# Kernel tuning notes

Measured on AMD Instinct MI355X. Metric: run time of the kernel, lower is better.

Reference implementation:

```python
import jax, jax.numpy as jnp
import numpy as np

SEQ, VOCAB, HID, OUT = 8192, 256, 2048, 256


def setup_inputs() -> dict:
    key = jax.random.key(0)
    ks = jax.random.split(key, 21)
    def lin(kw, fan_in, shape):
        return (jax.random.normal(kw, shape, dtype=jnp.float32) / np.sqrt(fan_in)).astype(jnp.float32)
    inp = {
        "x": jax.random.randint(ks[0], (SEQ, 1), 0, VOCAB, dtype=jnp.int64 if jax.config.read("jax_enable_x64") else jnp.int32),
        "emb": jax.random.normal(ks[1], (VOCAB, VOCAB), dtype=jnp.float32),
        "W_i": lin(ks[2], VOCAB, (VOCAB, HID)), "b_i": lin(ks[3], VOCAB, (HID,)),
        "U_i": lin(ks[4], HID, (HID, HID)),   "c_i": lin(ks[5], HID, (HID,)),
        "W_f": lin(ks[6], VOCAB, (VOCAB, HID)), "b_f": lin(ks[7], VOCAB, (HID,)),
        "U_f": lin(ks[8], HID, (HID, HID)),   "c_f": lin(ks[9], HID, (HID,)),
        "W_g": lin(ks[10], VOCAB, (VOCAB, HID)), "b_g": lin(ks[11], VOCAB, (HID,)),
        "U_g": lin(ks[12], HID, (HID, HID)),  "c_g": lin(ks[13], HID, (HID,)),
        "W_o": lin(ks[14], VOCAB, (VOCAB, HID)), "b_o": lin(ks[15], VOCAB, (HID,)),
        "U_o": lin(ks[16], HID, (HID, HID)),  "c_o": lin(ks[17], HID, (HID,)),
        "V_w": lin(ks[18], HID, (HID, OUT)),  "V_b": lin(ks[19], HID, (OUT,)),
    }
    return inp


def reference(x, emb, W_i, b_i, U_i, c_i, W_f, b_f, U_f, c_f,
              W_g, b_g, U_g, c_g, W_o, b_o, U_o, c_o, V_w, V_b):
    H = U_i.shape[0]
    # embedding lookup: (S,1) ids -> (S,1,V)
    x_emb = emb[x[:, 0]][:, None, :]
    # precompute all input projections (the W_* matmuls are time-independent)
    gi = x_emb @ W_i + b_i  # (S,1,H)
    gf = x_emb @ W_f + b_f
    gg = x_emb @ W_g + b_g
    go = x_emb @ W_o + b_o

    def step(carry, gates):
        h, c = carry  # (1,H) each
        zi, zf, zg, zo = gates
        i = jax.nn.sigmoid(zi + h @ U_i + c_i)
        f = jax.nn.sigmoid(zf + h @ U_f + c_f)
        g = jnp.tanh(zg + h @ U_g + c_g)
        o = jax.nn.sigmoid(zo + h @ U_o + c_o)
        c_new = f * c + i * g
        h_new = o * jnp.tanh(c_new)
        return (h_new, c_new), h_new

    h0 = jnp.zeros((1, H), dtype=x_emb.dtype)
    c0 = jnp.zeros((1, H), dtype=x_emb.dtype)
    (h_T, c_T), hs = jax.lax.scan(step, (h0, c0), (gi, gf, gg, go))
    out = hs @ V_w + V_b  # (S,1,OUT)
    return out, (jax.lax.stop_gradient(h_T), jax.lax.stop_gradient(c_T))
```

## Files before the change

kernel.cpp:

```cpp
#include <hip/hip_runtime.h>

#define SEQ   8192
#define VOCAB 256
#define HID   2048
#define ODIM  256
#define NBLK  256
#define NTHR  512
#define JPB   8

typedef unsigned int v4u __attribute__((ext_vector_type(4)));

__device__ __forceinline__ void ld32_coh_sync(const void* p, v4u& r0, v4u& r1) {
    asm volatile("global_load_dwordx4 %0, %2, off sc0 sc1\n\t"
                 "global_load_dwordx4 %1, %2, off offset:16 sc0 sc1\n\t"
                 "s_waitcnt vmcnt(0)"
                 : "=&v"(r0), "=&v"(r1) : "v"(p) : "memory");
}

__device__ __forceinline__ float fsigmoid(float x) {
    return __builtin_amdgcn_rcpf(1.f + __expf(-x));
}
__device__ __forceinline__ float ftanh(float x) {
    x = fminf(20.f, fmaxf(-20.f, x));
    float e = __expf(2.f * x);
    return (e - 1.f) * __builtin_amdgcn_rcpf(e + 1.f);
}

__device__ __forceinline__ float dpp_ror4(float v) {
    return __int_as_float(__builtin_amdgcn_update_dpp(
        0, __float_as_int(v), 0x124, 0xF, 0xF, false));
}
__device__ __forceinline__ float dpp_ror8(float v) {
    return __int_as_float(__builtin_amdgcn_update_dpp(
        0, __float_as_int(v), 0x128, 0xF, 0xF, false));
}

__global__ void k_zv(const float* __restrict__ emb, const float* __restrict__ W,
                     const float* __restrict__ bb, const float* __restrict__ cb,
                     float* __restrict__ Zv, int gate) {
    __shared__ float e[32][VOCAB];
    const int tid = threadIdx.x;
    const int vt = blockIdx.x, ct = blockIdx.y;
    for (int r = 0; r < 32; ++r)
        e[r][tid] = emb[(size_t)(vt * 32 + r) * VOCAB + tid];
    __syncthreads();
    const int j = ct * 256 + tid;
    const float bias = bb[j] + cb[j];
    float acc[32];
#pragma unroll
    for (int r = 0; r < 32; ++r) acc[r] = 0.f;
    for (int u = 0; u < VOCAB; ++u) {
        float w = W[(size_t)u * HID + j];
#pragma unroll
        for (int r = 0; r < 32; ++r) acc[r] += e[r][u] * w;
    }
    for (int r = 0; r < 32; ++r)
        Zv[(size_t)(vt * 32 + r) * (4 * HID) + (size_t)gate * HID + j] = acc[r] + bias;
}

__launch_bounds__(NTHR, 2)
__global__ void k_lstm(const float* __restrict__ Uii, const float* __restrict__ Uff,
                       const float* __restrict__ Ugg, const float* __restrict__ Uoo,
                       const float* __restrict__ Zv,  const int* __restrict__ x,
                       unsigned long long* pub, float* __restrict__ hs,
                       float* __restrict__ outTail) {
    __shared__ __align__(16) float hpad[128 * 20];
    __shared__ __align__(16) float scr2[2][32 * 36];

    const int tid  = threadIdx.x;
    const int b    = blockIdx.x;
    const int gate = tid & 3;
    const int rs   = tid >> 2;
    const int lane = tid & 63;
    const int wv   = tid >> 6;
    const int jg   = b * JPB + wv;

    const float* Ug = (gate == 0) ? Uii : (gate == 1) ? Uff : (gate == 2) ? Ugg : Uoo;

    float u[16][JPB];
#pragma unroll
    for (int r = 0; r < 16; ++r) {
        const float4* p = (const float4*)(Ug + (size_t)(rs * 16 + r) * HID + b * JPB);
        float4 a0 = p[0], a1 = p[1];
        u[r][0] = a0.x; u[r][1] = a0.y; u[r][2] = a0.z; u[r][3] = a0.w;
        u[r][4] = a1.x; u[r][5] = a1.y; u[r][6] = a1.z; u[r][7] = a1.w;
    }

    float4* hp4 = (float4*)hpad;
    float creg = 0.f;
    unsigned budget = 1u << 22;

    for (int t = 0; t < SEQ; ++t) {
        const int xt = x[t];
        float zx = Zv[(size_t)xt * (4 * HID) + (size_t)gate * HID + jg];

        float4 hv;
        if (t == 0) {
            hv = make_float4(0.f, 0.f, 0.f, 0.f);
        } else {
            const unsigned tgt = (unsigned)t;
            const unsigned long long* sl = pub + (size_t)(t & 1) * HID + tid * 4;
            v4u A0, A1;
            for (;;) {
                ld32_coh_sync(sl, A0, A1);
                if (((A0.y == tgt) & (A0.w == tgt) &
                     (A1.y == tgt) & (A1.w == tgt)) || budget == 0) break;
                --budget;
                __builtin_amdgcn_s_sleep(1);
            }
            hv.x = __uint_as_float(A0.x);
            hv.y = __uint_as_float(A0.z);
            hv.z = __uint_as_float(A1.x);
            hv.w = __uint_as_float(A1.z);
        }

        *(float4*)&hpad[(tid >> 2) * 20 + (tid & 3) * 4] = hv;
        __threadfence_block();

        float acc[JPB];
#pragma unroll
        for (int jj = 0; jj < JPB; ++jj) acc[jj] = 0.f;
#pragma unroll
        for (int k = 0; k < 4; ++k) {
            float4 h4 = hp4[rs * 5 + k];
            float hvv[4] = {h4.x, h4.y, h4.z, h4.w};
#pragma unroll
            for (int i = 0; i < 4; ++i)
#pragma unroll
                for (int jj = 0; jj < JPB; ++jj)
                    acc[jj] += hvv[i] * u[k * 4 + i][jj];
        }

#pragma unroll
        for (int jj = 0; jj < JPB; ++jj) {
            acc[jj] += dpp_ror4(acc[jj]);
            acc[jj] += dpp_ror8(acc[jj]);
        }
        if ((lane & 12) == 0) {
            const int chunk = wv * 4 + (lane >> 4);
            float* p = &scr2[t & 1][chunk * 36 + gate * JPB];
            *(float4*)(p)     = make_float4(acc[0], acc[1], acc[2], acc[3]);
            *(float4*)(p + 4) = make_float4(acc[4], acc[5], acc[6], acc[7]);
        }
        __syncthreads();

        {
            const int c = lane >> 2;
            const float* s = &scr2[t & 1][0];
            float z = s[c * 36 + gate * JPB + wv] +
                      s[(c + 16) * 36 + gate * JPB + wv];
            z += __shfl_xor(z, 4);
            z += __shfl_xor(z, 8);
            z += __shfl_xor(z, 16);
            z += __shfl_xor(z, 32);
            z += zx;
            float zi = __shfl(z, 0);
            float zf = __shfl(z, 1);
            float zg = __shfl(z, 2);
            float zo = __shfl(z, 3);
            float ig = fsigmoid(zi);
            float fg = fsigmoid(zf);
            float gg = ftanh(zg);
            float og = fsigmoid(zo);
            float cn = fg * creg + ig * gg;
            float hn = og * ftanh(cn);
            creg = cn;
            if (lane == 0) {
                unsigned long long pk =
                    ((unsigned long long)(unsigned)(t + 1) << 32) | __float_as_uint(hn);
                __hip_atomic_store(&pub[(size_t)((t + 1) & 1) * HID + jg], pk,
                                   __ATOMIC_RELAXED, __HIP_MEMORY_SCOPE_AGENT);
                hs[(size_t)t * HID + jg] = hn;
                if (t == SEQ - 1) { outTail[jg] = hn; outTail[HID + jg] = cn; }
            }
        }
    }
}

__global__ void k_out(const float* __restrict__ hs, const float* __restrict__ Vw,
                      const float* __restrict__ Vb, float* __restrict__ out) {
    __shared__ float tile[32][64];
    const int tid = threadIdx.x;
    const int t0 = blockIdx.x * 32;
    float acc[32];
#pragma unroll
    for (int r = 0; r < 32; ++r) acc[r] = 0.f;
    for (int k0 = 0; k0 < HID; k0 += 64) {
        {
            const int r = tid >> 3, kk = (tid & 7) * 8;
            const float4* p = (const float4*)(hs + (size_t)(t0 + r) * HID + k0 + kk);
            float4 a = p[0], bq = p[1];
            *(float4*)&tile[r][kk]     = a;
            *(float4*)&tile[r][kk + 4] = bq;
        }
        __syncthreads();
        for (int kk = 0; kk < 64; ++kk) {
            float w = Vw[(size_t)(k0 + kk) * ODIM + tid];
#pragma unroll
            for (int r = 0; r < 32; ++r) acc[r] += tile[r][kk] * w;
        }
        __syncthreads();
    }
    const float vb = Vb[tid];
    for (int r = 0; r < 32; ++r)
        out[(size_t)(t0 + r) * ODIM + tid] = acc[r] + vb;
}

extern "C" void kernel_launch(void* const* d_in, const int* in_sizes, int n_in,
                              void* d_out, int out_size, void* d_ws, size_t ws_size,
                              hipStream_t stream) {
    const int*   x   = (const int*)d_in[0];
    const float* emb = (const float*)d_in[1];
    const float* W[4] = {(const float*)d_in[2], (const float*)d_in[6],
                         (const float*)d_in[10], (const float*)d_in[14]};
    const float* B[4] = {(const float*)d_in[3], (const float*)d_in[7],
                         (const float*)d_in[11], (const float*)d_in[15]};
    const float* U[4] = {(const float*)d_in[4], (const float*)d_in[8],
                         (const float*)d_in[12], (const float*)d_in[16]};
    const float* C[4] = {(const float*)d_in[5], (const float*)d_in[9],
                         (const float*)d_in[13], (const float*)d_in[17]};
    const float* Vw = (const float*)d_in[18];
    const float* Vb = (const float*)d_in[19];
    float* out = (float*)d_out;

    float* ws = (float*)d_ws;
    float* Zv = ws;
    float* hs = Zv + (size_t)VOCAB * 4 * HID;
    unsigned long long* pub = (unsigned long long*)(hs + (size_t)SEQ * HID);

    for (int g = 0; g < 4; ++g)
        k_zv<<<dim3(8, 8), dim3(256), 0, stream>>>(emb, W[g], B[g], C[g], Zv, g);

    float* outTail = out + (size_t)SEQ * ODIM;
    const float *Ui = U[0], *Uf = U[1], *Ugp = U[2], *Uo = U[3];
    const float* Zvc = Zv; const int* xc = x;
    unsigned long long* pubc = pub; float* hsc = hs; float* ot = outTail;
    void* args[9] = {&Ui, &Uf, &Ugp, &Uo, &Zvc, &xc, &pubc, &hsc, &ot};
    hipLaunchCooperativeKernel((void*)k_lstm, dim3(NBLK), dim3(NTHR), args, 0, stream);

    k_out<<<dim3(256), dim3(256), 0, stream>>>(hs, Vw, Vb, out);
}
```

Baseline: 17.60 ms.

## Split publish slots into two halves and poll each half independently

Rearranges the per-step published hidden-state slots so each reader thread's four values sit in two 16-byte chunks in separate halves of the buffer, written by different waves. The spin loop now re-polls only the chunk that is still stale instead of reloading all 32 bytes, and alternates probes when both are stale. The intent is to cut coherent-load traffic and latency in the cross-block synchronisation of the sequential LSTM recurrence. In exchange the polling loop has more branching and the slot index mapping is harder to follow.

```diff
diff --git a/kernel.cpp b/kernel.cpp
--- a/kernel.cpp
+++ b/kernel.cpp
@@ -10,11 +10,18 @@
 
 typedef unsigned int v4u __attribute__((ext_vector_type(4)));
 
-__device__ __forceinline__ void ld32_coh_sync(const void* p, v4u& r0, v4u& r1) {
+__device__ __forceinline__ void ld16_coh_sync(const void* p, v4u& r) {
+    asm volatile("global_load_dwordx4 %0, %1, off sc0 sc1\n\t"
+                 "s_waitcnt vmcnt(0)"
+                 : "=&v"(r) : "v"(p) : "memory");
+}
+
+__device__ __forceinline__ void ld32_2q(const void* pE, const void* pO,
+                                        v4u& r0, v4u& r1) {
     asm volatile("global_load_dwordx4 %0, %2, off sc0 sc1\n\t"
-                 "global_load_dwordx4 %1, %2, off offset:16 sc0 sc1\n\t"
+                 "global_load_dwordx4 %1, %3, off sc0 sc1\n\t"
                  "s_waitcnt vmcnt(0)"
-                 : "=&v"(r0), "=&v"(r1) : "v"(p) : "memory");
+                 : "=&v"(r0), "=&v"(r1) : "v"(pE), "v"(pO) : "memory");
 }
 
 __device__ __forceinline__ float fsigmoid(float x) {
@@ -86,6 +93,8 @@
         u[r][4] = a1.x; u[r][5] = a1.y; u[r][6] = a1.z; u[r][7] = a1.w;
     }
 
+    const size_t pslot = (size_t)((wv & 2) ? 1024 : 0) + 4 * b + 2 * ((wv >> 2) & 1) + (wv & 1);
+
     float4* hp4 = (float4*)hpad;
     float creg = 0.f;
     unsigned budget = 1u << 22;
@@ -99,19 +108,33 @@
             hv = make_float4(0.f, 0.f, 0.f, 0.f);
         } else {
             const unsigned tgt = (unsigned)t;
-            const unsigned long long* sl = pub + (size_t)(t & 1) * HID + tid * 4;
-            v4u A0, A1;
-            for (;;) {
-                ld32_coh_sync(sl, A0, A1);
-                if (((A0.y == tgt) & (A0.w == tgt) &
-                     (A1.y == tgt) & (A1.w == tgt)) || budget == 0) break;
-                --budget;
-                __builtin_amdgcn_s_sleep(1);
+            const unsigned long long* slE = pub + (size_t)(t & 1) * 2048 + tid * 2;
+            const unsigned long long* slO = slE + 1024;
+            v4u Q0, Q1, A;
+            ld32_2q(slE, slO, Q0, Q1);
+            bool f0 = (Q0.y == tgt) & (Q0.w == tgt);
+            bool f1 = (Q1.y == tgt) & (Q1.w == tgt);
+            unsigned ph = 0;
+            while (!(f0 & f1) && budget != 0) {
+                if (!(f0 | f1)) __builtin_amdgcn_s_sleep(2);
+                --budget; ++ph;
+                const bool probe1 = f0 | ((!f0) & (!f1) & ((ph & 1u) != 0u));
+                const unsigned long long* pr = probe1 ? slO : slE;
+                ld16_coh_sync(pr, A);
+                const bool fresh = (A.y == tgt) & (A.w == tgt);
+                const bool c1 = fresh & probe1;
+                const bool c0 = fresh & (!probe1);
+                Q1.x = c1 ? A.x : Q1.x; Q1.y = c1 ? A.y : Q1.y;
+                Q1.z = c1 ? A.z : Q1.z; Q1.w = c1 ? A.w : Q1.w;
+                Q0.x = c0 ? A.x : Q0.x; Q0.y = c0 ? A.y : Q0.y;
+                Q0.z = c0 ? A.z : Q0.z; Q0.w = c0 ? A.w : Q0.w;
+                f1 = f1 | c1;
+                f0 = f0 | c0;
             }
-            hv.x = __uint_as_float(A0.x);
-            hv.y = __uint_as_float(A0.z);
-            hv.z = __uint_as_float(A1.x);
-            hv.w = __uint_as_float(A1.z);
+            hv.x = __uint_as_float(Q0.x);
+            hv.y = __uint_as_float(Q0.z);
+            hv.z = __uint_as_float(Q1.x);
+            hv.w = __uint_as_float(Q1.z);
         }
 
         *(float4*)&hpad[(tid >> 2) * 20 + (tid & 3) * 4] = hv;
@@ -168,7 +191,7 @@
             if (lane == 0) {
                 unsigned long long pk =
                     ((unsigned long long)(unsigned)(t + 1) << 32) | __float_as_uint(hn);
-                __hip_atomic_store(&pub[(size_t)((t + 1) & 1) * HID + jg], pk,
+                __hip_atomic_store(&pub[(size_t)((t + 1) & 1) * 2048 + pslot], pk,
                                    __ATOMIC_RELAXED, __HIP_MEMORY_SCOPE_AGENT);
                 hs[(size_t)t * HID + jg] = hn;
                 if (t == SEQ - 1) { outTail[jg] = hn; outTail[HID + jg] = cn; }
```

After: 17.03 ms. -3.2%, faster.

## Pipeline coherent flag polling with double-buffered loads and interleave publish slots

Applied to the files above, without the earlier changes.

Replaces the serial load-wait-sleep polling loop with inline-asm polling that keeps two pairs of coherent loads in flight, checking one while the next is already issued, and drops the s_sleep. The publish slot layout is permuted so each thread's four hidden values come from two separate 16-byte regions (even/odd halves), so the slots written by the eight waves of a block sit together. The aim is to cut the latency of the per-timestep cross-block barrier in the cooperative LSTM recurrence. In exchange it hardcodes VGPRs v40-v59 and SGPRs s84-s89 as clobbers, which may increase register pressure, and busy polling without sleep adds memory traffic.

```diff
diff --git a/kernel.cpp b/kernel.cpp
--- a/kernel.cpp
+++ b/kernel.cpp
@@ -8,15 +8,6 @@
 #define NTHR  512
 #define JPB   8
 
-typedef unsigned int v4u __attribute__((ext_vector_type(4)));
-
-__device__ __forceinline__ void ld32_coh_sync(const void* p, v4u& r0, v4u& r1) {
-    asm volatile("global_load_dwordx4 %0, %2, off sc0 sc1\n\t"
-                 "global_load_dwordx4 %1, %2, off offset:16 sc0 sc1\n\t"
-                 "s_waitcnt vmcnt(0)"
-                 : "=&v"(r0), "=&v"(r1) : "v"(p) : "memory");
-}
-
 __device__ __forceinline__ float fsigmoid(float x) {
     return __builtin_amdgcn_rcpf(1.f + __expf(-x));
 }
@@ -33,6 +24,87 @@
 __device__ __forceinline__ float dpp_ror8(float v) {
     return __int_as_float(__builtin_amdgcn_update_dpp(
         0, __float_as_int(v), 0x128, 0xF, 0xF, false));
+}
+
+__device__ __forceinline__ float4 poll_pipelined(const unsigned long long* slE,
+                                                 const unsigned long long* slO,
+                                                 unsigned tgt, unsigned& budget) {
+    const unsigned long long ea = (unsigned long long)(uintptr_t)slE;
+    const unsigned long long oa = (unsigned long long)(uintptr_t)slO;
+    unsigned elo = (unsigned)ea, ehi = (unsigned)(ea >> 32);
+    unsigned olo = (unsigned)oa, ohi = (unsigned)(oa >> 32);
+    unsigned o0, o1, o2, o3, budo;
+    asm volatile(
+        "v_mov_b32 v40, %[elo]\n\t"
+        "v_mov_b32 v41, %[ehi]\n\t"
+        "v_mov_b32 v42, %[olo]\n\t"
+        "v_mov_b32 v43, %[ohi]\n\t"
+        "v_readfirstlane_b32 s88, %[tgt]\n\t"
+        "v_readfirstlane_b32 s89, %[bud]\n\t"
+        "global_load_dwordx4 v[44:47], v[40:41], off sc0 sc1\n\t"
+        "global_load_dwordx4 v[48:51], v[42:43], off sc0 sc1\n\t"
+        "global_load_dwordx4 v[52:55], v[40:41], off sc0 sc1\n\t"
+        "global_load_dwordx4 v[56:59], v[42:43], off sc0 sc1\n\t"
+        "1:\n\t"
+        "s_waitcnt vmcnt(2)\n\t"
+        "v_cmp_eq_u32 vcc, s88, v45\n\t"
+        "s_mov_b64 s[84:85], vcc\n\t"
+        "v_cmp_eq_u32 vcc, s88, v47\n\t"
+        "s_and_b64 s[84:85], s[84:85], vcc\n\t"
+        "v_cmp_eq_u32 vcc, s88, v49\n\t"
+        "s_and_b64 s[84:85], s[84:85], vcc\n\t"
+        "v_cmp_eq_u32 vcc, s88, v51\n\t"
+        "s_and_b64 s[84:85], s[84:85], vcc\n\t"
+        "s_andn2_b64 s[86:87], exec, s[84:85]\n\t"
+        "s_cbranch_scc0 20f\n\t"
+        "global_load_dwordx4 v[44:47], v[40:41], off sc0 sc1\n\t"
+        "global_load_dwordx4 v[48:51], v[42:43], off sc0 sc1\n\t"
+        "s_waitcnt vmcnt(2)\n\t"
+        "v_cmp_eq_u32 vcc, s88, v53\n\t"
+        "s_mov_b64 s[84:85], vcc\n\t"
+        "v_cmp_eq_u32 vcc, s88, v55\n\t"
+        "s_and_b64 s[84:85], s[84:85], vcc\n\t"
+        "v_cmp_eq_u32 vcc, s88, v57\n\t"
+        "s_and_b64 s[84:85], s[84:85], vcc\n\t"
+        "v_cmp_eq_u32 vcc, s88, v59\n\t"
+        "s_and_b64 s[84:85], s[84:85], vcc\n\t"
+        "s_andn2_b64 s[86:87], exec, s[84:85]\n\t"
+        "s_cbranch_scc0 21f\n\t"
+        "global_load_dwordx4 v[52:55], v[40:41], off sc0 sc1\n\t"
+        "global_load_dwordx4 v[56:59], v[42:43], off sc0 sc1\n\t"
+        "s_cmp_eq_u32 s89, 0\n\t"
+        "s_cbranch_scc1 20f\n\t"
+        "s_sub_u32 s89, s89, 1\n\t"
+        "s_branch 1b\n\t"
+        "20:\n\t"
+        "s_waitcnt vmcnt(0)\n\t"
+        "v_mov_b32 %[o0], v44\n\t"
+        "v_mov_b32 %[o1], v46\n\t"
+        "v_mov_b32 %[o2], v48\n\t"
+        "v_mov_b32 %[o3], v50\n\t"
+        "s_branch 99f\n\t"
+        "21:\n\t"
+        "s_waitcnt vmcnt(0)\n\t"
+        "v_mov_b32 %[o0], v52\n\t"
+        "v_mov_b32 %[o1], v54\n\t"
+        "v_mov_b32 %[o2], v56\n\t"
+        "v_mov_b32 %[o3], v58\n\t"
+        "99:\n\t"
+        "v_mov_b32 %[budo], s89\n\t"
+        : [o0] "=&v"(o0), [o1] "=&v"(o1), [o2] "=&v"(o2), [o3] "=&v"(o3),
+          [budo] "=&v"(budo)
+        : [elo] "v"(elo), [ehi] "v"(ehi), [olo] "v"(olo), [ohi] "v"(ohi),
+          [tgt] "v"(tgt), [bud] "v"(budget)
+        : "v40","v41","v42","v43","v44","v45","v46","v47","v48","v49",
+          "v50","v51","v52","v53","v54","v55","v56","v57","v58","v59",
+          "s84","s85","s86","s87","s88","s89","vcc","scc","memory");
+    budget = budo;
+    float4 hv;
+    hv.x = __uint_as_float(o0);
+    hv.y = __uint_as_float(o1);
+    hv.z = __uint_as_float(o2);
+    hv.w = __uint_as_float(o3);
+    return hv;
 }
 
 __global__ void k_zv(const float* __restrict__ emb, const float* __restrict__ W,
@@ -86,6 +158,8 @@
         u[r][4] = a1.x; u[r][5] = a1.y; u[r][6] = a1.z; u[r][7] = a1.w;
     }
 
+    const size_t pslot = (size_t)((wv & 2) ? 1024 : 0) + 4 * b + 2 * ((wv >> 2) & 1) + (wv & 1);
+
     float4* hp4 = (float4*)hpad;
     float creg = 0.f;
     unsigned budget = 1u << 22;
@@ -98,20 +172,9 @@
         if (t == 0) {
             hv = make_float4(0.f, 0.f, 0.f, 0.f);
         } else {
-            const unsigned tgt = (unsigned)t;
-            const unsigned long long* sl = pub + (size_t)(t & 1) * HID + tid * 4;
-            v4u A0, A1;
-            for (;;) {
-                ld32_coh_sync(sl, A0, A1);
-                if (((A0.y == tgt) & (A0.w == tgt) &
-                     (A1.y == tgt) & (A1.w == tgt)) || budget == 0) break;
-                --budget;
-                __builtin_amdgcn_s_sleep(1);
-            }
-            hv.x = __uint_as_float(A0.x);
-            hv.y = __uint_as_float(A0.z);
-            hv.z = __uint_as_float(A1.x);
-            hv.w = __uint_as_float(A1.z);
+            const unsigned long long* slE = pub + (size_t)(t & 1) * 2048 + tid * 2;
+            const unsigned long long* slO = slE + 1024;
+            hv = poll_pipelined(slE, slO, (unsigned)t, budget);
         }
 
         *(float4*)&hpad[(tid >> 2) * 20 + (tid & 3) * 4] = hv;
@@ -168,7 +231,7 @@
             if (lane == 0) {
                 unsigned long long pk =
                     ((unsigned long long)(unsigned)(t + 1) << 32) | __float_as_uint(hn);
-                __hip_atomic_store(&pub[(size_t)((t + 1) & 1) * HID + jg], pk,
+                __hip_atomic_store(&pub[(size_t)((t + 1) & 1) * 2048 + pslot], pk,
                                    __ATOMIC_RELAXED, __HIP_MEMORY_SCOPE_AGENT);
                 hs[(size_t)t * HID + jg] = hn;
                 if (t == SEQ - 1) { outTail[jg] = hn; outTail[HID + jg] = cn; }
@@ -236,7 +299,7 @@
     const float* Zvc = Zv; const int* xc = x;
     unsigned long long* pubc = pub; float* hsc = hs; float* ot = outTail;
     void* args[9] = {&Ui, &Uf, &Ugp, &Uo, &Zvc, &xc, &pubc, &hsc, &ot};
-    hipLaunchCooperativeKernel((void*)k_lstm, dim3(NBLK), dim3(NTHR), args, 0, stream);
+    (void)hipLaunchCooperativeKernel((void*)k_lstm, dim3(NBLK), dim3(NTHR), args, 0, stream);
 
     k_out<<<dim3(256), dim3(256), 0, stream>>>(hs, Vw, Vb, out);
 }
```

New measurement: 17.61 ms. No clear change (+0.1%).
